# Performance work log

Measured on AMD Instinct MI355X. Metric: run time of the kernel, lower is better.

Reference implementation:

```python
import jax, jax.numpy as jnp
import numpy as np

EPS = 1e-8
PAD = -4294967295.0  # -2**32 + 1


def dice(x, alpha):
    # Dice activation: batch-normalize over all axes except features, sigmoid gate.
    mean = jnp.mean(x, axis=(0, 1), keepdims=True)
    var = jnp.var(x, axis=(0, 1), keepdims=True)
    xn = (x - mean) * jax.lax.rsqrt(var + EPS)
    p = jax.nn.sigmoid(xn)
    return p * x + alpha * (1.0 - p) * x


def setup_inputs() -> dict:
    key = jax.random.key(0)
    ks = jax.random.split(key, 12)
    B, T, D = 2048, 200, 64
    H1, H2 = 80, 40
    queries = jax.random.normal(ks[0], (B, 1, D), dtype=jnp.float32)
    keys = jax.random.normal(ks[1], (B, T, D), dtype=jnp.float32)
    mask = jax.random.randint(ks[2], (B, T), 0, 2).astype(jnp.bool_)
    s1 = 1.0 / np.sqrt(4 * D)
    s2 = 1.0 / np.sqrt(H1)
    s3 = 1.0 / np.sqrt(H2)
    W1 = jax.random.normal(ks[3], (4 * D, H1), dtype=jnp.float32) * s1
    b1 = jnp.zeros((H1,), dtype=jnp.float32)
    a1 = jnp.zeros((H1,), dtype=jnp.float32)
    W2 = jax.random.normal(ks[4], (H1, H2), dtype=jnp.float32) * s2
    b2 = jnp.zeros((H2,), dtype=jnp.float32)
    a2 = jnp.zeros((H2,), dtype=jnp.float32)
    W3 = jax.random.normal(ks[5], (H2, 1), dtype=jnp.float32) * s3
    b3 = jnp.zeros((1,), dtype=jnp.float32)
    return {"queries": queries, "keys": keys, "mask": mask,
            "W1": W1, "b1": b1, "a1": a1,
            "W2": W2, "b2": b2, "a2": a2,
            "W3": W3, "b3": b3}


def reference(queries, keys, mask, W1, b1, a1, W2, b2, a2, W3, b3):
    # queries: [B,1,D], keys: [B,T,D], mask: [B,T] bool
    q = jnp.broadcast_to(queries, keys.shape)  # tile over T
    x = jnp.concatenate([q, keys, q - keys, q * keys], axis=-1)  # [B,T,4D]
    x = dice(jnp.einsum('btf,fh->bth', x, W1) + b1, a1)          # [B,T,80]
    x = dice(jnp.einsum('btf,fh->bth', x, W2) + b2, a2)          # [B,T,40]
    scores = (jnp.einsum('btf,fo->bto', x, W3) + b3)[..., 0]     # [B,T]
    scores = jnp.where(mask, scores, PAD)
    w = jax.nn.softmax(scores, axis=-1)                           # [B,T]
    out = jnp.einsum('btd,bt->bd', keys, w)                       # [B,D]
    return out
```

## Files before the change

### kernel.cpp

```cpp
#include <hip/hip_runtime.h>
#include <hip/hip_fp16.h>
#include <math.h>

#define NB 2048
#define T 200
#define D 64
#define H1 80
#define H2 40
#define NROWS (NB * T)
#define NBLK3 (NROWS / 128)
#define EPSV 1e-8f
#define PADV -4294967295.0f

typedef _Float16 f16x8 __attribute__((ext_vector_type(8)));
typedef float f32x4 __attribute__((ext_vector_type(4)));

#define Z1H_OFF   0ull
#define Z2H_OFF   65536000ull
#define QT_OFF    98304000ull
#define RED1_OFF  98959360ull
#define RED2_OFF  100270080ull
#define FIN1_OFF  101294080ull
#define FIN2_OFF  101294720ull

__device__ __forceinline__ float dice_f(float z, float m, float r, float a) {
  const float xn = (z - m) * r;
  const float p = 1.f / (1.f + expf(-xn));
  return z * (p + a * (1.f - p));
}

__global__ __launch_bounds__(128) void k0_qt(
    const float* __restrict__ qry, const float* __restrict__ W1,
    const float* __restrict__ b1, float* __restrict__ qt)
{
  const int b = blockIdx.x, tid = threadIdx.x;
  __shared__ float qsh[D];
  if (tid < D) qsh[tid] = qry[b * D + tid];
  __syncthreads();
  if (tid < H1) {
    float s = b1[tid];
    #pragma unroll 8
    for (int f = 0; f < D; ++f)
      s += qsh[f] * (W1[f * H1 + tid] + W1[(2 * D + f) * H1 + tid]);
    qt[b * H1 + tid] = s;
  }
}

__global__ __launch_bounds__(512) void k1_gemm(
    const float* __restrict__ keys, const float* __restrict__ W1,
    const float* __restrict__ qry, const float* __restrict__ qt,
    __half* __restrict__ z1h, float* __restrict__ red1p)
{
  const int b = blockIdx.x, tid = threadIdx.x;
  const int lane = tid & 63, w = tid >> 6;
  __shared__ __align__(16) _Float16 ksh[208][72];
  __shared__ __align__(16) _Float16 wsh[80][72];
  __shared__ float qsh[D];
  __shared__ float qtsh[H1];
  __shared__ float bsum[H1], bsq[H1];

  if (tid < D) qsh[tid] = qry[b * D + tid];
  if (tid < H1) { qtsh[tid] = qt[b * H1 + tid]; bsum[tid] = 0.f; bsq[tid] = 0.f; }
  __syncthreads();

  for (int idx = tid; idx < D * H1; idx += 512) {
    const int f = idx / H1, h = idx - f * H1;
    const float v = W1[(D + f) * H1 + h] - W1[(2 * D + f) * H1 + h]
                  + qsh[f] * W1[(3 * D + f) * H1 + h];
    wsh[h][f] = (_Float16)v;
  }
  const float2* ksrc = (const float2*)(keys + (size_t)b * T * D);
  for (int idx = tid; idx < (T * D) / 2; idx += 512) {
    const int t = idx >> 5, f2 = idx & 31;
    const float2 kv = ksrc[idx];
    union { _Float16 h[2]; unsigned u; } pk;
    pk.h[0] = (_Float16)kv.x; pk.h[1] = (_Float16)kv.y;
    *(unsigned*)&ksh[t][f2 * 2] = pk.u;
  }
  __syncthreads();

  const int r = lane & 15, g = lane >> 4;
  float sum[5] = {0.f,0.f,0.f,0.f,0.f}, sq[5] = {0.f,0.f,0.f,0.f,0.f};

  for (int strip = w; strip < 13; strip += 8) {
    const int m0 = strip * 16;
    const f16x8 fa0 = *(const f16x8*)&ksh[m0 + r][g * 8];
    const f16x8 fa1 = *(const f16x8*)&ksh[m0 + r][32 + g * 8];
    #pragma unroll
    for (int n = 0; n < 5; ++n) {
      const f16x8 fb0 = *(const f16x8*)&wsh[n * 16 + r][g * 8];
      const f16x8 fb1 = *(const f16x8*)&wsh[n * 16 + r][32 + g * 8];
      f32x4 c = {0.f, 0.f, 0.f, 0.f};
      c = __builtin_amdgcn_mfma_f32_16x16x32_f16(fa0, fb0, c, 0, 0, 0);
      c = __builtin_amdgcn_mfma_f32_16x16x32_f16(fa1, fb1, c, 0, 0, 0);
      const int col = n * 16 + r;
      const float qv = qtsh[col];
      #pragma unroll
      for (int j = 0; j < 4; ++j) {
        const int row = m0 + g * 4 + j;
        if (row < T) {
          const float o = c[j] + qv;
          z1h[((size_t)b * T + row) * H1 + col] = __float2half(o);
          sum[n] += o; sq[n] += o * o;
        }
      }
    }
  }
  #pragma unroll
  for (int n = 0; n < 5; ++n) {
    float s = sum[n], q2 = sq[n];
    s += __shfl_xor(s, 16);  s += __shfl_xor(s, 32);
    q2 += __shfl_xor(q2, 16); q2 += __shfl_xor(q2, 32);
    if (g == 0) {
      atomicAdd(&bsum[n * 16 + r], s);
      atomicAdd(&bsq[n * 16 + r], q2);
    }
  }
  __syncthreads();
  if (tid < H1) {
    red1p[(size_t)b * 160 + tid]      = bsum[tid];
    red1p[(size_t)b * 160 + H1 + tid] = bsq[tid];
  }
}

__global__ __launch_bounds__(256) void k_fin_par(
    const float* __restrict__ redp, float* __restrict__ fin, int H, int P)
{
  const int h = blockIdx.x, tid = threadIdx.x;
  const int S = 2 * H;
  float s = 0.f, q = 0.f;
  for (int p = tid; p < P; p += 256) {
    s += redp[(size_t)p * S + h];
    q += redp[(size_t)p * S + H + h];
  }
  #pragma unroll
  for (int o = 32; o > 0; o >>= 1) { s += __shfl_xor(s, o); q += __shfl_xor(q, o); }
  __shared__ float ssh[4], qsh[4];
  const int wid = tid >> 6;
  if ((tid & 63) == 0) { ssh[wid] = s; qsh[wid] = q; }
  __syncthreads();
  if (tid == 0) {
    const float st = (ssh[0] + ssh[1]) + (ssh[2] + ssh[3]);
    const float qt = (qsh[0] + qsh[1]) + (qsh[2] + qsh[3]);
    const float n = (float)NROWS;
    const float mean = st / n;
    const float var = qt / n - mean * mean;
    fin[h] = mean;
    fin[H + h] = rsqrtf(var + EPSV);
  }
}

__global__ __launch_bounds__(512) void k3_z2(
    const __half* __restrict__ z1h, const float* __restrict__ W2,
    const float* __restrict__ b2, const float* __restrict__ a1,
    const float* __restrict__ fin1, __half* __restrict__ z2h,
    float* __restrict__ red2p)
{
  const int blk = blockIdx.x, tid = threadIdx.x;
  const int lane = tid & 63, w = tid >> 6;
  const int r0 = blk * 128;
  __shared__ __align__(16) _Float16 h1sh[128][104];
  __shared__ __align__(16) _Float16 w2t[48][104];
  __shared__ float m1[H1], r1[H1], al1[H1];
  __shared__ float b2sh[48];
  __shared__ float bsum[48], bsq[48];

  if (tid < H1) { m1[tid] = fin1[tid]; r1[tid] = fin1[H1 + tid]; al1[tid] = a1[tid]; }
  if (tid < 48) { b2sh[tid] = (tid < H2) ? b2[tid] : 0.f; bsum[tid] = 0.f; bsq[tid] = 0.f; }
  for (int idx = tid; idx < (48 * 104) / 2; idx += 512)
    ((unsigned*)w2t)[idx] = 0u;
  for (int idx = tid; idx < 128 * 8; idx += 512) {
    const int n = idx >> 3, c = idx & 7;
    *(unsigned*)((char*)&h1sh[n][80] + c * 4) = 0u;
  }
  __syncthreads();

  for (int idx = tid; idx < H1 * H2; idx += 512) {
    const int k = idx / H2, h2 = idx - k * H2;
    w2t[h2][k] = (_Float16)W2[idx];
  }
  const uint2* z1v = (const uint2*)(z1h + (size_t)r0 * H1);
  for (int idx = tid; idx < (128 * H1) / 4; idx += 512) {
    const int n = idx / 20, c4 = (idx - n * 20) * 4;
    const uint2 raw = z1v[idx];
    union { uint2 u; __half h[4]; } in; in.u = raw;
    union { _Float16 h[4]; unsigned long long u; } outp;
    #pragma unroll
    for (int j = 0; j < 4; ++j) {
      const int hh = c4 + j;
      const float z = __half2float(in.h[j]);
      outp.h[j] = (_Float16)dice_f(z, m1[hh], r1[hh], al1[hh]);
    }
    *(unsigned long long*)&h1sh[n][c4] = outp.u;
  }
  __syncthreads();

  const int r = lane & 15, g = lane >> 4;
  const int m0 = w * 16;
  const f16x8 fa0 = *(const f16x8*)&h1sh[m0 + r][g * 8];
  const f16x8 fa1 = *(const f16x8*)&h1sh[m0 + r][32 + g * 8];
  const f16x8 fa2 = *(const f16x8*)&h1sh[m0 + r][64 + g * 8];
  float sum[3] = {0.f,0.f,0.f}, sq[3] = {0.f,0.f,0.f};
  #pragma unroll
  for (int n = 0; n < 3; ++n) {
    const f16x8 fb0 = *(const f16x8*)&w2t[n * 16 + r][g * 8];
    const f16x8 fb1 = *(const f16x8*)&w2t[n * 16 + r][32 + g * 8];
    const f16x8 fb2 = *(const f16x8*)&w2t[n * 16 + r][64 + g * 8];
    f32x4 c = {0.f, 0.f, 0.f, 0.f};
    c = __builtin_amdgcn_mfma_f32_16x16x32_f16(fa0, fb0, c, 0, 0, 0);
    c = __builtin_amdgcn_mfma_f32_16x16x32_f16(fa1, fb1, c, 0, 0, 0);
    c = __builtin_amdgcn_mfma_f32_16x16x32_f16(fa2, fb2, c, 0, 0, 0);
    const int col = n * 16 + r;
    if (col < H2) {
      const float bb = b2sh[col];
      #pragma unroll
      for (int j = 0; j < 4; ++j) {
        const int row = m0 + g * 4 + j;
        const float o = c[j] + bb;
        z2h[((size_t)r0 + row) * H2 + col] = __float2half(o);
        sum[n] += o; sq[n] += o * o;
      }
    }
  }
  #pragma unroll
  for (int n = 0; n < 3; ++n) {
    float s = sum[n], q2 = sq[n];
    s += __shfl_xor(s, 16);  s += __shfl_xor(s, 32);
    q2 += __shfl_xor(q2, 16); q2 += __shfl_xor(q2, 32);
    const int col = n * 16 + r;
    if (g == 0 && col < H2) {
      atomicAdd(&bsum[col], s);
      atomicAdd(&bsq[col], q2);
    }
  }
  __syncthreads();
  if (tid < H2) {
    red2p[(size_t)blk * 80 + tid]      = bsum[tid];
    red2p[(size_t)blk * 80 + H2 + tid] = bsq[tid];
  }
}

__global__ __launch_bounds__(512, 4) void k5_out(
    const __half* __restrict__ z2h, const float* __restrict__ keys,
    const int* __restrict__ mask, const float* __restrict__ a2,
    const float* __restrict__ fin2, const float* __restrict__ W3,
    const float* __restrict__ b3, float* __restrict__ out)
{
  const int b = blockIdx.x, tid = threadIdx.x;
  __shared__ float h2sh[T][H2 + 1];
  __shared__ float w3sh[H2], m2[H2], r2[H2], al2[H2];
  __shared__ float ssh[T];
  __shared__ float red[16];
  __shared__ float osh[8][D];

  if (tid < H2) {
    w3sh[tid] = W3[tid];
    m2[tid] = fin2[tid];
    r2[tid] = fin2[H2 + tid];
    al2[tid] = a2[tid];
  }
  __syncthreads();
  const __half2* z2v = (const __half2*)(z2h + (size_t)b * T * H2);
  for (int idx = tid; idx < (T * H2) / 2; idx += 512) {
    const int n = idx / 20, hh = (idx - n * 20) * 2;
    const float2 zf = __half22float2(z2v[idx]);
    h2sh[n][hh]     = dice_f(zf.x, m2[hh],     r2[hh],     al2[hh]);
    h2sh[n][hh + 1] = dice_f(zf.y, m2[hh + 1], r2[hh + 1], al2[hh + 1]);
  }
  __syncthreads();

  float s = -INFINITY;
  if (tid < T) {
    s = b3[0];
    #pragma unroll 8
    for (int f = 0; f < H2; ++f) s = fmaf(h2sh[tid][f], w3sh[f], s);
    if (!mask[b * T + tid]) s = PADV;
  }
  float v = s;
  #pragma unroll
  for (int o = 32; o > 0; o >>= 1) v = fmaxf(v, __shfl_xor(v, o, 64));
  const int lane = tid & 63, wid = tid >> 6;
  if (lane == 0) red[wid] = v;
  __syncthreads();
  float m = red[0];
  #pragma unroll
  for (int w = 1; w < 8; ++w) m = fmaxf(m, red[w]);
  float e = 0.f;
  if (tid < T) { e = expf(s - m); ssh[tid] = e; }
  float v2 = e;
  #pragma unroll
  for (int o = 32; o > 0; o >>= 1) v2 += __shfl_xor(v2, o, 64);
  if (lane == 0) red[8 + wid] = v2;
  __syncthreads();
  float denom = 0.f;
  #pragma unroll
  for (int w = 0; w < 8; ++w) denom += red[8 + w];
  const float inv = 1.f / denom;

  const int dd = tid & 63, tg = tid >> 6;
  float p = 0.f;
  for (int t = tg; t < T; t += 8)
    p = fmaf(ssh[t], keys[((size_t)(b * T) + t) * D + dd], p);
  osh[tg][dd] = p * inv;
  __syncthreads();
  if (tid < D) {
    float o = 0.f;
    #pragma unroll
    for (int w = 0; w < 8; ++w) o += osh[w][tid];
    out[(size_t)b * D + tid] = o;
  }
}

extern "C" void kernel_launch(void* const* d_in, const int* in_sizes, int n_in,
                              void* d_out, int out_size, void* d_ws, size_t ws_size,
                              hipStream_t stream)
{
  const float* qry  = (const float*)d_in[0];
  const float* keys = (const float*)d_in[1];
  const int*   mask = (const int*)d_in[2];
  const float* W1   = (const float*)d_in[3];
  const float* b1   = (const float*)d_in[4];
  const float* a1   = (const float*)d_in[5];
  const float* W2   = (const float*)d_in[6];
  const float* b2   = (const float*)d_in[7];
  const float* a2   = (const float*)d_in[8];
  const float* W3   = (const float*)d_in[9];
  const float* b3   = (const float*)d_in[10];
  float* out = (float*)d_out;
  char* ws = (char*)d_ws;

  __half* z1h  = (__half*)(ws + Z1H_OFF);
  __half* z2h  = (__half*)(ws + Z2H_OFF);
  float* qt    = (float*)(ws + QT_OFF);
  float* red1p = (float*)(ws + RED1_OFF);
  float* red2p = (float*)(ws + RED2_OFF);
  float* fin1  = (float*)(ws + FIN1_OFF);
  float* fin2  = (float*)(ws + FIN2_OFF);

  k0_qt<<<NB, 128, 0, stream>>>(qry, W1, b1, qt);
  k1_gemm<<<NB, 512, 0, stream>>>(keys, W1, qry, qt, z1h, red1p);
  k_fin_par<<<H1, 256, 0, stream>>>(red1p, fin1, H1, NB);
  k3_z2<<<NBLK3, 512, 0, stream>>>(z1h, W2, b2, a1, fin1, z2h, red2p);
  k_fin_par<<<H2, 256, 0, stream>>>(red2p, fin2, H2, NBLK3);
  k5_out<<<NB, 512, 0, stream>>>(z2h, keys, mask, a2, fin2, W3, b3, out);
}
```

Baseline: 320.3 us.

## Split k1 GEMM into two half-sequence blocks per batch with float4 loads

The first-layer GEMM kernel now launches two blocks per batch element, each handling 100 of the 200 timesteps. This halves the keys shared-memory tile and gives each of 7 waves a single strip. Per-block partial statistics are written per half-block, so the reduction kernel now reads twice as many partials. Keys are loaded as float4 and launch bounds request higher occupancy for k1 and k3. In exchange, each block recomputes the folded W1 weight tile, doubling that setup work, and one wave per block sits idle.

```diff
diff --git a/kernel.cpp b/kernel.cpp
--- a/kernel.cpp
+++ b/kernel.cpp
@@ -8,6 +8,7 @@
 #define H1 80
 #define H2 40
 #define NROWS (NB * T)
+#define NBLK1 (NB * 2)
 #define NBLK3 (NROWS / 128)
 #define EPSV 1e-8f
 #define PADV -4294967295.0f
@@ -19,9 +20,9 @@
 #define Z2H_OFF   65536000ull
 #define QT_OFF    98304000ull
 #define RED1_OFF  98959360ull
-#define RED2_OFF  100270080ull
-#define FIN1_OFF  101294080ull
-#define FIN2_OFF  101294720ull
+#define RED2_OFF  101580800ull
+#define FIN1_OFF  102604800ull
+#define FIN2_OFF  102605440ull
 
 __device__ __forceinline__ float dice_f(float z, float m, float r, float a) {
   const float xn = (z - m) * r;
@@ -46,14 +47,15 @@
   }
 }
 
-__global__ __launch_bounds__(512) void k1_gemm(
+__global__ __launch_bounds__(512, 8) void k1_gemm(
     const float* __restrict__ keys, const float* __restrict__ W1,
     const float* __restrict__ qry, const float* __restrict__ qt,
     __half* __restrict__ z1h, float* __restrict__ red1p)
 {
-  const int b = blockIdx.x, tid = threadIdx.x;
+  const int blk = blockIdx.x, tid = threadIdx.x;
+  const int b = blk >> 1, half = blk & 1;
   const int lane = tid & 63, w = tid >> 6;
-  __shared__ __align__(16) _Float16 ksh[208][72];
+  __shared__ __align__(16) _Float16 ksh[112][72];
   __shared__ __align__(16) _Float16 wsh[80][72];
   __shared__ float qsh[D];
   __shared__ float qtsh[H1];
@@ -69,21 +71,22 @@
                   + qsh[f] * W1[(3 * D + f) * H1 + h];
     wsh[h][f] = (_Float16)v;
   }
-  const float2* ksrc = (const float2*)(keys + (size_t)b * T * D);
-  for (int idx = tid; idx < (T * D) / 2; idx += 512) {
-    const int t = idx >> 5, f2 = idx & 31;
-    const float2 kv = ksrc[idx];
-    union { _Float16 h[2]; unsigned u; } pk;
+  const float4* ksrc = (const float4*)(keys + ((size_t)b * T + half * 100) * D);
+  for (int idx = tid; idx < 100 * D / 4; idx += 512) {
+    const int t = idx >> 4, f4 = idx & 15;
+    const float4 kv = ksrc[idx];
+    union { _Float16 h[4]; unsigned long long u; } pk;
     pk.h[0] = (_Float16)kv.x; pk.h[1] = (_Float16)kv.y;
-    *(unsigned*)&ksh[t][f2 * 2] = pk.u;
+    pk.h[2] = (_Float16)kv.z; pk.h[3] = (_Float16)kv.w;
+    *(unsigned long long*)&ksh[t][f4 * 4] = pk.u;
   }
   __syncthreads();
 
   const int r = lane & 15, g = lane >> 4;
   float sum[5] = {0.f,0.f,0.f,0.f,0.f}, sq[5] = {0.f,0.f,0.f,0.f,0.f};
 
-  for (int strip = w; strip < 13; strip += 8) {
-    const int m0 = strip * 16;
+  if (w < 7) {
+    const int m0 = w * 16;
     const f16x8 fa0 = *(const f16x8*)&ksh[m0 + r][g * 8];
     const f16x8 fa1 = *(const f16x8*)&ksh[m0 + r][32 + g * 8];
     #pragma unroll
@@ -98,9 +101,9 @@
       #pragma unroll
       for (int j = 0; j < 4; ++j) {
         const int row = m0 + g * 4 + j;
-        if (row < T) {
+        if (row < 100) {
           const float o = c[j] + qv;
-          z1h[((size_t)b * T + row) * H1 + col] = __float2half(o);
+          z1h[((size_t)b * T + half * 100 + row) * H1 + col] = __float2half(o);
           sum[n] += o; sq[n] += o * o;
         }
       }
@@ -111,15 +114,15 @@
     float s = sum[n], q2 = sq[n];
     s += __shfl_xor(s, 16);  s += __shfl_xor(s, 32);
     q2 += __shfl_xor(q2, 16); q2 += __shfl_xor(q2, 32);
-    if (g == 0) {
+    if (g == 0 && w < 7) {
       atomicAdd(&bsum[n * 16 + r], s);
       atomicAdd(&bsq[n * 16 + r], q2);
     }
   }
   __syncthreads();
   if (tid < H1) {
-    red1p[(size_t)b * 160 + tid]      = bsum[tid];
-    red1p[(size_t)b * 160 + H1 + tid] = bsq[tid];
+    red1p[(size_t)blk * 160 + tid]      = bsum[tid];
+    red1p[(size_t)blk * 160 + H1 + tid] = bsq[tid];
   }
 }
 
@@ -150,7 +153,7 @@
   }
 }
 
-__global__ __launch_bounds__(512) void k3_z2(
+__global__ __launch_bounds__(512, 8) void k3_z2(
     const __half* __restrict__ z1h, const float* __restrict__ W2,
     const float* __restrict__ b2, const float* __restrict__ a1,
     const float* __restrict__ fin1, __half* __restrict__ z2h,
@@ -338,8 +341,8 @@
   float* fin2  = (float*)(ws + FIN2_OFF);
 
   k0_qt<<<NB, 128, 0, stream>>>(qry, W1, b1, qt);
-  k1_gemm<<<NB, 512, 0, stream>>>(keys, W1, qry, qt, z1h, red1p);
-  k_fin_par<<<H1, 256, 0, stream>>>(red1p, fin1, H1, NB);
+  k1_gemm<<<NBLK1, 512, 0, stream>>>(keys, W1, qry, qt, z1h, red1p);
+  k_fin_par<<<H1, 256, 0, stream>>>(red1p, fin1, H1, NBLK1);
   k3_z2<<<NBLK3, 512, 0, stream>>>(z1h, W2, b2, a1, fin1, z2h, red2p);
   k_fin_par<<<H2, 256, 0, stream>>>(red2p, fin2, H2, NBLK3);
   k5_out<<<NB, 512, 0, stream>>>(z2h, keys, mask, a2, fin2, W3, b3, out);
```

New measurement: 323.6 us. Within noise of the previous version (+1.0%).
